# Kernel tuning notes

Measured on AMD Instinct MI355X. Metric: run time of the kernel, lower is better.

The kernel has to match this reference:

```python
import jax, jax.numpy as jnp
import numpy as np

B, L, D, H = 2, 2048, 1024, 16
HD = D // H  # 64


def rotate_half(x):
    x1, x2 = x[..., : x.shape[-1] // 2], x[..., x.shape[-1] // 2 :]
    return jnp.concatenate([-x2, x1], axis=-1)


def apply_rope(x, cos, sin):
    # x: (B, H, L, HD); cos/sin: (1, L, HD)
    c = cos[:, None, : x.shape[2], :]
    s = sin[:, None, : x.shape[2], :]
    return x * c + rotate_half(x) * s


def setup_inputs() -> dict:
    key = jax.random.key(0)
    ks = jax.random.split(key, 16)
    query = jax.random.normal(ks[0], (B, L, D), jnp.float32)
    k_in = jax.random.normal(ks[1], (B, L, D), jnp.float32)
    v_in = jax.random.normal(ks[2], (B, L, D), jnp.float32)
    key_padding_mask = jax.random.uniform(ks[3], (B, L)) < 0.2
    # genuine RoPE tables
    inv_freq = 1.0 / (10000.0 ** (jnp.arange(0, HD, 2, dtype=jnp.float32) / HD))
    ang = jnp.arange(L, dtype=jnp.float32)[:, None] * inv_freq[None, :]  # (L, HD/2)
    ang = jnp.concatenate([ang, ang], axis=-1)  # (L, HD)
    rope_cos = jnp.cos(ang)[None]  # (1, L, HD)
    rope_sin = jnp.sin(ang)[None]
    scale = 0.02
    Wq = jax.random.normal(ks[4], (D, D), jnp.float32) * scale
    bq = jnp.zeros((D,), jnp.float32)
    Wk = jax.random.normal(ks[5], (D, D), jnp.float32) * scale
    bk = jnp.zeros((D,), jnp.float32)
    Wv = jax.random.normal(ks[6], (D, D), jnp.float32) * scale
    bv = jnp.zeros((D,), jnp.float32)
    Wg = jax.random.normal(ks[7], (D, D), jnp.float32) * scale  # init zeros in torch; random for grad coverage
    bg = jnp.ones((D,), jnp.float32)
    Wo = jax.random.normal(ks[8], (D, D), jnp.float32) * scale
    bo = jnp.zeros((D,), jnp.float32)
    return dict(query=query, key=k_in, value=v_in, key_padding_mask=key_padding_mask,
                rope_cos=rope_cos, rope_sin=rope_sin,
                Wq=Wq, bq=bq, Wk=Wk, bk=bk, Wv=Wv, bv=bv,
                Wg=Wg, bg=bg, Wo=Wo, bo=bo)


def reference(query, key, value, key_padding_mask, rope_cos, rope_sin,
              Wq, bq, Wk, bk, Wv, bv, Wg, bg, Wo, bo):
    Bq, Lq, _ = query.shape
    Lk = key.shape[1]
    # torch Linear: x @ W.T + b
    Q = (query @ Wq.T + bq).reshape(Bq, Lq, H, HD).transpose(0, 2, 1, 3)
    K = (key @ Wk.T + bk).reshape(Bq, Lk, H, HD).transpose(0, 2, 1, 3)
    V = (value @ Wv.T + bv).reshape(Bq, Lk, H, HD).transpose(0, 2, 1, 3)
    K = apply_rope(K, rope_cos, rope_sin)
    Q = apply_rope(Q, rope_cos, rope_sin)
    scale = 1.0 / jnp.sqrt(jnp.asarray(HD, query.dtype))
    scores = jnp.einsum('bhqd,bhkd->bhqk', Q, K) * scale
    allow = ~key_padding_mask[:, None, None, :]  # (B,1,1,Lk): True = attend
    scores = jnp.where(allow, scores, -jnp.inf)
    attn = jax.nn.softmax(scores, axis=-1)
    out = jnp.einsum('bhqk,bhkd->bhqd', attn, V)
    out = jnp.nan_to_num(out, nan=0.0)
    out = out.transpose(0, 2, 1, 3).reshape(Bq, Lq, D)
    gate = jax.nn.sigmoid(query @ Wg.T + bg)
    out = out * gate
    out = out @ Wo.T + bo
    return out
```

## Files before the change

kernel.cpp:

```cpp
#include <hip/hip_runtime.h>
#include <hip/hip_bf16.h>
#include <cstdint>


constexpr int NB = 2, NL = 2048, ND = 1024, NH = 16, NHD = 64;
constexpr int NM = NB * NL;

typedef __bf16 bf16_t;
typedef __bf16 bf16x8 __attribute__((ext_vector_type(8)));
typedef __bf16 bf16x4 __attribute__((ext_vector_type(4)));
typedef float f32x4 __attribute__((ext_vector_type(4)));
typedef float f32x16 __attribute__((ext_vector_type(16)));
typedef unsigned int uint2v __attribute__((ext_vector_type(2)));

typedef const __attribute__((address_space(1))) void* gas_ptr;
typedef __attribute__((address_space(3))) void* las_ptr;

__device__ __forceinline__ void async_load16(const void* g, void* l) {
  __builtin_amdgcn_global_load_lds((gas_ptr)g, (las_ptr)l, 16, 0, 0);
}

__device__ __forceinline__ unsigned cvtpk_bf16(float lo, float hi) {
  unsigned r;
  asm("v_cvt_pk_bf16_f32 %0, %1, %2" : "=v"(r) : "v"(lo), "v"(hi));
  return r;
}

__device__ __forceinline__ void pl32_swap(unsigned& a, unsigned& b) {
#if __has_builtin(__builtin_amdgcn_permlane32_swap)
  uint2v r = __builtin_amdgcn_permlane32_swap(a, b, false, false);
  a = r.x; b = r.y;
#else
  asm volatile("v_permlane32_swap_b32 %0, %1" : "+v"(a), "+v"(b));
#endif
}

struct CvtArgs {
  const float* s[8];
  bf16_t* d[8];
};
__global__ __launch_bounds__(256) void cvt8_kernel(CvtArgs a) {
  int y = blockIdx.y;
  int n4 = (y < 3) ? (NM * ND / 4) : (ND * ND / 4);
  const float* src = a.s[y];
  bf16_t* dst = a.d[y];
  for (int i = blockIdx.x * 256 + threadIdx.x; i < n4; i += gridDim.x * 256) {
    float4 v = ((const float4*)src)[i];
    bf16x4 o;
    o[0] = (bf16_t)v.x; o[1] = (bf16_t)v.y; o[2] = (bf16_t)v.z; o[3] = (bf16_t)v.w;
    ((bf16x4*)dst)[i] = o;
  }
}

template <int MODE>
__global__ __launch_bounds__(256) void gemm_kernel(
    const bf16_t* __restrict__ Aq, const bf16_t* __restrict__ Ak, const bf16_t* __restrict__ Av,
    const bf16_t* __restrict__ W0, const bf16_t* __restrict__ W1,
    const bf16_t* __restrict__ W2, const bf16_t* __restrict__ W3,
    const float* __restrict__ b0, const float* __restrict__ b1,
    const float* __restrict__ b2, const float* __restrict__ b3,
    const float* __restrict__ ctab, const float* __restrict__ stab,
    bf16_t* __restrict__ Qr, bf16_t* __restrict__ Kr, bf16_t* __restrict__ Vt,
    bf16_t* __restrict__ Gb, float* __restrict__ Out) {
  __shared__ __align__(16) bf16_t lA[2][128 * 64];
  __shared__ __align__(16) bf16_t lB[2][128 * 64];
  const int tid = threadIdx.x, lane = tid & 63, w = tid >> 6;
  const int wm = w >> 1, wn = w & 1;
  const int lr = lane & 15, lg = lane >> 4;

  const int lin = blockIdx.x;
  const int xcd = lin & 7, idx = lin >> 3;
  constexpr int G = (MODE == 1) ? 4 : 1;
  const int ntile = xcd * G + (idx & (G - 1));
  const int mtile = idx / G;

  const bf16_t* Asrc;
  const bf16_t* Wsrc;
  int nofs, t = 0;
  if constexpr (MODE == 1) {
    t = ntile >> 3;
    Asrc = (t == 1) ? Ak : (t == 2) ? Av : Aq;
    Wsrc = (t == 0) ? W0 : (t == 1) ? W1 : (t == 2) ? W2 : W3;
    nofs = (ntile & 7) * 128;
  } else {
    Asrc = Aq; Wsrc = W0; nofs = ntile * 128;
  }
  const bf16_t* Ablk = Asrc + mtile * 128 * ND;
  const bf16_t* Wblk = Wsrc + nofs * ND;

  f32x4 acc[4][4];
#pragma unroll
  for (int i = 0; i < 4; ++i)
#pragma unroll
    for (int j = 0; j < 4; ++j)
#pragma unroll
      for (int k = 0; k < 4; ++k) acc[i][j][k] = 0.f;

  auto STAGE = [&](int b, int kb) {
#pragma unroll
    for (int p = 0; p < 4; ++p) {
      int q = w * 256 + p * 64 + lane;
      int r = q >> 3, c = q & 7;
      int cs = c ^ (r & 7);
      async_load16(Ablk + r * ND + kb * 64 + cs * 8, &lA[b][(w * 256 + p * 64) * 8]);
      async_load16(Wblk + r * ND + kb * 64 + cs * 8, &lB[b][(w * 256 + p * 64) * 8]);
    }
  };
  auto COMPUTE = [&](int b) {
    const bf16_t* pA = lA[b];
    const bf16_t* pB = lB[b];
#pragma unroll
    for (int ks = 0; ks < 2; ++ks) {
      bf16x8 af[4], bfr[4];
#pragma unroll
      for (int i = 0; i < 4; ++i) {
        int ra = wm * 64 + i * 16 + lr;
        int ca = (ks * 4 + lg) ^ (ra & 7);
        af[i] = *(const bf16x8*)(pA + ra * 64 + ca * 8);
        int rb = wn * 64 + i * 16 + lr;
        int cb = (ks * 4 + lg) ^ (rb & 7);
        bfr[i] = *(const bf16x8*)(pB + rb * 64 + cb * 8);
      }
#pragma unroll
      for (int i = 0; i < 4; ++i)
#pragma unroll
        for (int j = 0; j < 4; ++j)
          acc[i][j] = __builtin_amdgcn_mfma_f32_16x16x32_bf16(af[i], bfr[j], acc[i][j], 0, 0, 0);
    }
  };

  STAGE(0, 0);
  __syncthreads();
  int buf = 0;
  for (int kb = 0; kb < 15; ++kb) {
    STAGE(buf ^ 1, kb + 1);
    COMPUTE(buf);
    __syncthreads();
    buf ^= 1;
  }
  COMPUTE(buf);

  if constexpr (MODE == 0) {
#pragma unroll
    for (int j = 0; j < 4; ++j) {
      int nn = ntile * 128 + wn * 64 + j * 16 + lr;
      float bias = b0[nn];
#pragma unroll
      for (int i = 0; i < 4; ++i)
#pragma unroll
        for (int rg = 0; rg < 4; ++rg) {
          int mm = mtile * 128 + wm * 64 + i * 16 + lg * 4 + rg;
          Out[mm * ND + nn] = acc[i][j][rg] + bias;
        }
    }
  } else {
    const int fbase = nofs + wn * 64;
    const int h = fbase >> 6;
    if (t < 2) {
      bf16_t* dst = (t == 0) ? Qr : Kr;
      const float* bias = (t == 0) ? b0 : b1;
      const float qs = (t == 0) ? 0.18033688011112042f : 1.0f;
#pragma unroll
      for (int i = 0; i < 4; ++i)
#pragma unroll
        for (int rg = 0; rg < 4; ++rg) {
          int mm = mtile * 128 + wm * 64 + i * 16 + lg * 4 + rg;
          int bb = mm >> 11, l = mm & (NL - 1);
          bf16_t* rowp = dst + ((bb * NH + h) * NL + l) * NHD;
          const float* crow = ctab + l * NHD;
          const float* srow = stab + l * NHD;
#pragma unroll
          for (int j = 0; j < 2; ++j) {
            int dlo = j * 16 + lr, dhi = dlo + 32;
            float xlo = acc[i][j][rg] + bias[fbase + dlo];
            float xhi = acc[i][j + 2][rg] + bias[fbase + dhi];
            float olo = (xlo * crow[dlo] - xhi * srow[dlo]) * qs;
            float ohi = (xhi * crow[dhi] + xlo * srow[dhi]) * qs;
            rowp[dlo] = (bf16_t)olo;
            rowp[dhi] = (bf16_t)ohi;
          }
        }
    } else if (t == 2) {
#pragma unroll
      for (int i = 0; i < 4; ++i) {
        int mmb = mtile * 128 + wm * 64 + i * 16 + lg * 4;
        int bb = mmb >> 11, l0 = mmb & (NL - 1);
#pragma unroll
        for (int j = 0; j < 4; ++j) {
          int d = j * 16 + lr;
          float bias = b2[fbase + d];
          unsigned u01 = cvtpk_bf16(acc[i][j][0] + bias, acc[i][j][1] + bias);
          unsigned u23 = cvtpk_bf16(acc[i][j][2] + bias, acc[i][j][3] + bias);
          unsigned long long pk = (unsigned long long)u01 | ((unsigned long long)u23 << 32);
          *(unsigned long long*)(Vt + ((bb * NH + h) * NHD + d) * NL + l0) = pk;
        }
      }
    } else {
#pragma unroll
      for (int i = 0; i < 4; ++i)
#pragma unroll
        for (int rg = 0; rg < 4; ++rg) {
          int mm = mtile * 128 + wm * 64 + i * 16 + lg * 4 + rg;
#pragma unroll
          for (int j = 0; j < 4; ++j) {
            int f = fbase + j * 16 + lr;
            Gb[mm * ND + f] = (bf16_t)(acc[i][j][rg] + b3[f]);
          }
        }
    }
  }
}

__global__ __launch_bounds__(256) void attn_kernel(
    const bf16_t* __restrict__ Qr, const bf16_t* __restrict__ Kr, const bf16_t* __restrict__ Vt,
    const int* __restrict__ mask, const bf16_t* __restrict__ Gb, bf16_t* __restrict__ X) {
  __shared__ __align__(16) bf16_t lK[2][128 * 64];
  __shared__ __align__(16) bf16_t lV[2][64 * 128];

  int lin = blockIdx.y * gridDim.x + blockIdx.x;
  int swz = (lin & 7) * 64 + (lin >> 3);
  const int qb = swz & 15, bh = swz >> 4;
  const int bb = bh >> 4, h = bh & 15;

  const int tid = threadIdx.x, lane = tid & 63, w = tid >> 6;
  const int ql = lane & 31, hi = lane >> 5;

  const bf16_t* Kbh = Kr + bh * NL * NHD;
  const bf16_t* Vbh = Vt + bh * NHD * NL;
  const int q = qb * 128 + w * 32 + ql;

  const bf16_t* Qp = Qr + (bh * NL + q) * NHD + 8 * hi;
  bf16x8 qf[4];
#pragma unroll
  for (int c = 0; c < 4; ++c) qf[c] = *(const bf16x8*)(Qp + 16 * c);
  bf16x8 qf5 = {};
  qf5[0] = (bf16_t)(hi ? 0.f : 1.f);

  f32x16 acc[2];
#pragma unroll
  for (int dt = 0; dt < 2; ++dt)
#pragma unroll
    for (int r = 0; r < 16; ++r) acc[dt][r] = 0.f;
  float lrun = 0.f;

  const bf16_t* gsrc[8];
#pragma unroll
  for (int j = 0; j < 8; ++j) {
    if (j < 4) {
      int u = j * 256 + tid;
      int r = u >> 3, c = u & 7, cs = c ^ (r & 7);
      gsrc[j] = Kbh + r * NHD + cs * 8;
    } else {
      int v = (j - 4) * 256 + tid;
      int r = v >> 4, c = v & 15, cs = (c & 8) | ((c & 7) ^ (r & 7));
      gsrc[j] = Vbh + r * NL + cs * 8;
    }
  }
  auto STAGE = [&](int b) {
#pragma unroll
    for (int j = 0; j < 8; ++j) {
      if (j < 4) {
        async_load16(gsrc[j], &lK[b][(j * 256 + tid) * 8]);
        gsrc[j] += 128 * NHD;
      } else {
        async_load16(gsrc[j], &lV[b][((j - 4) * 256 + tid) * 8]);
        gsrc[j] += 128;
      }
    }
  };

  unsigned rdK[2][4], rdV[2][4];
#pragma unroll
  for (int t2 = 0; t2 < 2; ++t2)
#pragma unroll
    for (int c = 0; c < 4; ++c) {
      unsigned un = ((2 * c + hi) ^ (ql & 7)) * 16;
      rdK[t2][c] = (32 * t2 + ql) * 128 + un;
      rdV[t2][c] = (32 * t2 + ql) * 256 + un;
    }
  const char* lKc = (const char*)lK;
  const char* lVc = (const char*)lV;

  STAGE(0);
  int mv0 = mask[bb * NL + lane];
  int mv1 = mask[bb * NL + 64 + lane];
  __syncthreads();

  auto BODY = [&](int buf, int t) {
    int nmv0 = 0, nmv1 = 0;
    if (t < 15) {
      STAGE(buf ^ 1);
      nmv0 = mask[bb * NL + (t + 1) * 128 + lane];
      nmv1 = mask[bb * NL + (t + 1) * 128 + 64 + lane];
    }
    unsigned long long bmA = __ballot(mv0 != 0);
    unsigned long long bmB = __ballot(mv1 != 0);
    unsigned mws[4] = {(unsigned)bmA, (unsigned)(bmA >> 32),
                       (unsigned)bmB, (unsigned)(bmB >> 32)};
    bf16x8 kf5[4];
#pragma unroll
    for (int g = 0; g < 4; ++g) {
      float bv = ((mws[g] >> ql) & 1u) ? -1008.f : -8.f;
      bf16x8 z = {};
      z[0] = (bf16_t)(hi ? 0.f : bv);
      kf5[g] = z;
    }
    float ts[16];
#pragma unroll
    for (int hh = 0; hh < 2; ++hh) {
      f32x16 st[2];
      __builtin_amdgcn_s_setprio(1);
#pragma unroll
      for (int t2 = 0; t2 < 2; ++t2) {
        f32x16 s;
#pragma unroll
        for (int r = 0; r < 16; ++r) s[r] = 0.f;
#pragma unroll
        for (int c = 0; c < 4; ++c) {
          bf16x8 kf = *(const bf16x8*)(lKc + rdK[t2][c] + buf * 16384 + hh * 8192);
          s = __builtin_amdgcn_mfma_f32_32x32x16_bf16(kf, qf[c], s, 0, 0, 0);
        }
        s = __builtin_amdgcn_mfma_f32_32x32x16_bf16(kf5[hh * 2 + t2], qf5, s, 0, 0, 0);
        st[t2] = s;
      }
      __builtin_amdgcn_s_setprio(0);

#pragma unroll
      for (int t2 = 0; t2 < 2; ++t2)
#pragma unroll
        for (int r = 0; r < 16; ++r) st[t2][r] = exp2f(st[t2][r]);
#pragma unroll
      for (int r = 0; r < 16; ++r) {
        float v = st[0][r] + st[1][r];
        if (hh == 0) ts[r] = v; else ts[r] += v;
      }

      unsigned wds[2][4][2];
#pragma unroll
      for (int t2 = 0; t2 < 2; ++t2)
#pragma unroll
        for (int r1 = 0; r1 < 4; ++r1) {
          wds[t2][r1][0] = cvtpk_bf16(st[t2][4 * r1 + 0], st[t2][4 * r1 + 1]);
          wds[t2][r1][1] = cvtpk_bf16(st[t2][4 * r1 + 2], st[t2][4 * r1 + 3]);
        }
      bf16x8 pf[4];
#pragma unroll
      for (int kc = 0; kc < 4; ++kc) {
        int t2 = kc >> 1, r1a = 2 * (kc & 1);
        unsigned a0 = wds[t2][r1a][0], b0 = wds[t2][r1a + 1][0];
        unsigned a1 = wds[t2][r1a][1], b1 = wds[t2][r1a + 1][1];
        pl32_swap(a0, b0);
        pl32_swap(a1, b1);
        union { unsigned u[4]; bf16x8 v; } uu;
        uu.u[0] = a0; uu.u[1] = a1; uu.u[2] = b0; uu.u[3] = b1;
        pf[kc] = uu.v;
      }

      __builtin_amdgcn_s_setprio(1);
#pragma unroll
      for (int dt = 0; dt < 2; ++dt) {
        f32x16 a = acc[dt];
#pragma unroll
        for (int kc = 0; kc < 4; ++kc) {
          bf16x8 vf = *(const bf16x8*)(lVc + rdV[dt][kc] + buf * 16384 + hh * 128);
          a = __builtin_amdgcn_mfma_f32_32x32x16_bf16(vf, pf[kc], a, 0, 0, 0);
        }
        acc[dt] = a;
      }
      __builtin_amdgcn_s_setprio(0);
    }
#pragma unroll
    for (int off = 8; off > 0; off >>= 1)
#pragma unroll
      for (int r = 0; r < 8; ++r)
        if (r < off) ts[r] += ts[r + off];
    lrun += ts[0];
    __syncthreads();
    mv0 = nmv0;
    mv1 = nmv1;
  };

  for (int tt = 0; tt < 8; ++tt) {
    BODY(0, 2 * tt);
    BODY(1, 2 * tt + 1);
  }

  float lt = lrun + __shfl_xor(lrun, 32, 64);
  float rinv = lt > 0.f ? 1.f / lt : 0.f;
  const int rowbase = (bb * NL + q) * ND + h * NHD;
#pragma unroll
  for (int dt = 0; dt < 2; ++dt)
#pragma unroll
    for (int r1 = 0; r1 < 4; ++r1) {
      int dbase = 32 * dt + 8 * r1 + 4 * hi;
      bf16x4 g4 = *(const bf16x4*)(Gb + rowbase + dbase);
      bf16x4 o;
#pragma unroll
      for (int j = 0; j < 4; ++j) {
        float gate = 1.f / (1.f + exp2f(-1.44269504f * (float)g4[j]));
        o[j] = (bf16_t)(acc[dt][4 * r1 + j] * rinv * gate);
      }
      *(bf16x4*)(X + rowbase + dbase) = o;
    }
}

extern "C" void kernel_launch(void* const* d_in, const int* in_sizes, int n_in,
                              void* d_out, int out_size, void* d_ws, size_t ws_size,
                              hipStream_t stream) {
  const float* query = (const float*)d_in[0];
  const float* key   = (const float*)d_in[1];
  const float* value = (const float*)d_in[2];
  const int*   maskp = (const int*)d_in[3];
  const float* rcos  = (const float*)d_in[4];
  const float* rsin  = (const float*)d_in[5];
  const float* Wq = (const float*)d_in[6];  const float* bq = (const float*)d_in[7];
  const float* Wk = (const float*)d_in[8];  const float* bk = (const float*)d_in[9];
  const float* Wv = (const float*)d_in[10]; const float* bv = (const float*)d_in[11];
  const float* Wg = (const float*)d_in[12]; const float* bg = (const float*)d_in[13];
  const float* Wo = (const float*)d_in[14]; const float* bo = (const float*)d_in[15];

  constexpr size_t MB = 1ull << 20;
  char* ws = (char*)d_ws;
  bf16_t* qbb = (bf16_t*)(ws + 0 * MB);
  bf16_t* kbb = (bf16_t*)(ws + 8 * MB);
  bf16_t* vbb = (bf16_t*)(ws + 16 * MB);
  bf16_t* wqb = (bf16_t*)(ws + 24 * MB);
  bf16_t* wkb = (bf16_t*)(ws + 26 * MB);
  bf16_t* wvb = (bf16_t*)(ws + 28 * MB);
  bf16_t* wgb = (bf16_t*)(ws + 30 * MB);
  bf16_t* wob = (bf16_t*)(ws + 32 * MB);
  bf16_t* Qr  = (bf16_t*)(ws + 34 * MB);
  bf16_t* Kr  = (bf16_t*)(ws + 42 * MB);
  bf16_t* Vt  = (bf16_t*)(ws + 50 * MB);
  bf16_t* Gb  = (bf16_t*)(ws + 58 * MB);
  bf16_t* Xb  = (bf16_t*)(ws + 74 * MB);

  CvtArgs ca;
  ca.s[0] = query; ca.d[0] = qbb;
  ca.s[1] = key;   ca.d[1] = kbb;
  ca.s[2] = value; ca.d[2] = vbb;
  ca.s[3] = Wq;    ca.d[3] = wqb;
  ca.s[4] = Wk;    ca.d[4] = wkb;
  ca.s[5] = Wv;    ca.d[5] = wvb;
  ca.s[6] = Wg;    ca.d[6] = wgb;
  ca.s[7] = Wo;    ca.d[7] = wob;
  cvt8_kernel<<<dim3(1024, 8), 256, 0, stream>>>(ca);

  gemm_kernel<1><<<1024, 256, 0, stream>>>(
      qbb, kbb, vbb, wqb, wkb, wvb, wgb, bq, bk, bv, bg, rcos, rsin,
      Qr, Kr, Vt, Gb, nullptr);

  attn_kernel<<<dim3(16, 32), 256, 0, stream>>>(Qr, Kr, Vt, maskp, Gb, Xb);

  gemm_kernel<0><<<256, 256, 0, stream>>>(
      Xb, nullptr, nullptr, wob, nullptr, nullptr, nullptr,
      bo, nullptr, nullptr, nullptr, nullptr, nullptr,
      nullptr, nullptr, nullptr, nullptr, (float*)d_out);
}
```

Before: 152.8 us.

## Use 256x256-tile 8-wave pipelined GEMM for fused QKV/gate projection

Replaces the 128x128-tile, 4-wave projection GEMM with a 256x256-tile, 512-thread kernel using 128KB of dynamic LDS. Each of the 256 blocks handles a quarter-output slice for one of the Q/K/V/gate projections. Loads are staged in half-tiles interleaved with MFMA work, with explicit vmcnt waits, barriers and s_setprio raising wave priority around the MFMA bursts. The larger tile doubles reuse of global loads per output and cuts block count to one per CU. The cost is higher register and LDS pressure and more complex synchronization. The output-projection GEMM is split into its own simplified kernel with unchanged math.

```diff
diff --git a/kernel.cpp b/kernel.cpp
--- a/kernel.cpp
+++ b/kernel.cpp
@@ -52,8 +52,7 @@
   }
 }
 
-template <int MODE>
-__global__ __launch_bounds__(256) void gemm_kernel(
+__global__ __launch_bounds__(512, 2) void gemm8_kernel(
     const bf16_t* __restrict__ Aq, const bf16_t* __restrict__ Ak, const bf16_t* __restrict__ Av,
     const bf16_t* __restrict__ W0, const bf16_t* __restrict__ W1,
     const bf16_t* __restrict__ W2, const bf16_t* __restrict__ W3,
@@ -61,7 +60,178 @@
     const float* __restrict__ b2, const float* __restrict__ b3,
     const float* __restrict__ ctab, const float* __restrict__ stab,
     bf16_t* __restrict__ Qr, bf16_t* __restrict__ Kr, bf16_t* __restrict__ Vt,
-    bf16_t* __restrict__ Gb, float* __restrict__ Out) {
+    bf16_t* __restrict__ Gb) {
+  extern __shared__ __align__(16) bf16_t smem[];
+  bf16_t* lA = smem;
+  bf16_t* lB = smem + 32768;
+
+  const int tid = threadIdx.x, lane = tid & 63, w = tid >> 6;
+  const int wm = w >> 2, wn = w & 3;
+  const int lr = lane & 15, lg = lane >> 4;
+
+  const int lin = blockIdx.x;
+  const int xcd = lin & 7, idx = lin >> 3;
+  const int nt = xcd * 2 + (idx & 1);
+  const int mt = idx >> 1;
+  const int t = nt >> 2;
+  const bf16_t* Asrc = (t == 1) ? Ak : (t == 2) ? Av : Aq;
+  const bf16_t* Wsrc = (t == 0) ? W0 : (t == 1) ? W1 : (t == 2) ? W2 : W3;
+  const int nbase = (nt & 3) * 256;
+
+  const int srow = lane >> 3;
+  const int gcol = ((lane & 7) ^ srow) * 8;
+
+  auto stageA = [&](int buf, int hf, int kt) {
+#pragma unroll
+    for (int jj = 0; jj < 2; ++jj) {
+      int slot = jj * 8 + w;
+      int r = slot * 8 + srow;
+      async_load16(Asrc + (size_t)(mt * 256 + hf * 128 + r) * ND + kt * 64 + gcol,
+                   lA + (buf * 2 + hf) * 8192 + slot * 512);
+    }
+  };
+  auto stageB = [&](int buf, int hf, int kt) {
+#pragma unroll
+    for (int jj = 0; jj < 2; ++jj) {
+      int slot = jj * 8 + w;
+      int r = slot * 8 + srow;
+      async_load16(Wsrc + (size_t)(nbase + hf * 128 + r) * ND + kt * 64 + gcol,
+                   lB + (buf * 2 + hf) * 8192 + slot * 512);
+    }
+  };
+
+  f32x4 acc[8][4];
+#pragma unroll
+  for (int i = 0; i < 8; ++i)
+#pragma unroll
+    for (int j = 0; j < 4; ++j)
+#pragma unroll
+      for (int k = 0; k < 4; ++k) acc[i][j][k] = 0.f;
+
+  stageA(0, 0, 0); stageA(0, 1, 0); stageB(0, 0, 0); stageB(0, 1, 0);
+  stageB(1, 0, 1); stageB(1, 1, 1);
+  asm volatile("s_waitcnt vmcnt(4)" ::: "memory");
+  __builtin_amdgcn_s_barrier();
+
+  const bf16_t* Ab[2] = { lA + wm * 8192, lA + (2 + wm) * 8192 };
+  const bf16_t* Bb[2] = { lB + (wn >> 1) * 8192 + (wn & 1) * 4096,
+                          lB + (2 + (wn >> 1)) * 8192 + (wn & 1) * 4096 };
+
+  for (int j = 0; j < 8; ++j) {
+#pragma unroll
+    for (int hp = 0; hp < 2; ++hp) {
+      const bf16_t* Ap = Ab[hp];
+      const bf16_t* Bp = Bb[hp];
+      bf16x8 bfr[4][2];
+#pragma unroll
+      for (int p = 0; p < 4; ++p) {
+        bf16x8 af[2][2];
+#pragma unroll
+        for (int mi = 0; mi < 2; ++mi)
+#pragma unroll
+          for (int ks = 0; ks < 2; ++ks)
+            af[mi][ks] = *(const bf16x8*)(Ap + ((p * 2 + mi) * 16 + lr) * 64 +
+                                          ((ks * 4 + lg) ^ (lr & 7)) * 8);
+        if (p == 0) {
+#pragma unroll
+          for (int nj = 0; nj < 4; ++nj)
+#pragma unroll
+            for (int ks = 0; ks < 2; ++ks)
+              bfr[nj][ks] = *(const bf16x8*)(Bp + (nj * 16 + lr) * 64 +
+                                             ((ks * 4 + lg) ^ (lr & 7)) * 8);
+        }
+        if (hp == 0) {
+          if (p == 0) stageA(1, 0, 2 * j + 1);
+          if (p == 1) { stageA(1, 1, 2 * j + 1); if (j < 7) stageB(0, 0, 2 * j + 2); }
+          if (p == 2) { if (j < 7) stageB(0, 1, 2 * j + 2); }
+        } else if (j < 7) {
+          if (p == 0) stageA(0, 0, 2 * j + 2);
+          if (p == 1) { stageA(0, 1, 2 * j + 2); stageB(1, 0, 2 * j + 3); }
+          if (p == 2) stageB(1, 1, 2 * j + 3);
+        }
+        __builtin_amdgcn_s_barrier();
+        __builtin_amdgcn_s_setprio(1);
+#pragma unroll
+        for (int mi = 0; mi < 2; ++mi)
+#pragma unroll
+          for (int nj = 0; nj < 4; ++nj)
+#pragma unroll
+            for (int ks = 0; ks < 2; ++ks)
+              acc[p * 2 + mi][nj] = __builtin_amdgcn_mfma_f32_16x16x32_bf16(
+                  af[mi][ks], bfr[nj][ks], acc[p * 2 + mi][nj], 0, 0, 0);
+        __builtin_amdgcn_s_setprio(0);
+        if (p == 3) {
+          if (hp == 0) {
+            if (j < 7) { asm volatile("s_waitcnt vmcnt(4)" ::: "memory"); }
+            else       { asm volatile("s_waitcnt vmcnt(0)" ::: "memory"); }
+          } else if (j < 7) {
+            asm volatile("s_waitcnt vmcnt(4)" ::: "memory");
+          }
+        }
+        __builtin_amdgcn_s_barrier();
+      }
+    }
+  }
+
+  const int fbase = nbase + wn * 64;
+  const int h = fbase >> 6;
+  if (t < 2) {
+    bf16_t* dst = (t == 0) ? Qr : Kr;
+    const float* bias = (t == 0) ? b0 : b1;
+    const float qs = (t == 0) ? 0.18033688011112042f : 1.0f;
+#pragma unroll
+    for (int i = 0; i < 8; ++i)
+#pragma unroll
+      for (int rg = 0; rg < 4; ++rg) {
+        int mm = mt * 256 + wm * 128 + i * 16 + lg * 4 + rg;
+        int bb = mm >> 11, l = mm & (NL - 1);
+        bf16_t* rowp = dst + ((bb * NH + h) * NL + l) * NHD;
+        const float* crow = ctab + l * NHD;
+        const float* srw = stab + l * NHD;
+#pragma unroll
+        for (int nj = 0; nj < 2; ++nj) {
+          int dlo = nj * 16 + lr, dhi = dlo + 32;
+          float xlo = acc[i][nj][rg] + bias[fbase + dlo];
+          float xhi = acc[i][nj + 2][rg] + bias[fbase + dhi];
+          float olo = (xlo * crow[dlo] - xhi * srw[dlo]) * qs;
+          float ohi = (xhi * crow[dhi] + xlo * srw[dhi]) * qs;
+          rowp[dlo] = (bf16_t)olo;
+          rowp[dhi] = (bf16_t)ohi;
+        }
+      }
+  } else if (t == 2) {
+#pragma unroll
+    for (int i = 0; i < 8; ++i) {
+      int mmb = mt * 256 + wm * 128 + i * 16 + lg * 4;
+      int bb = mmb >> 11, l0 = mmb & (NL - 1);
+#pragma unroll
+      for (int nj = 0; nj < 4; ++nj) {
+        int d = nj * 16 + lr;
+        float bias = b2[fbase + d];
+        unsigned u01 = cvtpk_bf16(acc[i][nj][0] + bias, acc[i][nj][1] + bias);
+        unsigned u23 = cvtpk_bf16(acc[i][nj][2] + bias, acc[i][nj][3] + bias);
+        unsigned long long pk = (unsigned long long)u01 | ((unsigned long long)u23 << 32);
+        *(unsigned long long*)(Vt + ((bb * NH + h) * NHD + d) * NL + l0) = pk;
+      }
+    }
+  } else {
+#pragma unroll
+    for (int i = 0; i < 8; ++i)
+#pragma unroll
+      for (int rg = 0; rg < 4; ++rg) {
+        int mm = mt * 256 + wm * 128 + i * 16 + lg * 4 + rg;
+#pragma unroll
+        for (int nj = 0; nj < 4; ++nj) {
+          int f = fbase + nj * 16 + lr;
+          Gb[mm * ND + f] = (bf16_t)(acc[i][nj][rg] + b3[f]);
+        }
+      }
+  }
+}
+
+__global__ __launch_bounds__(256) void gemm_out_kernel(
+    const bf16_t* __restrict__ A, const bf16_t* __restrict__ W,
+    const float* __restrict__ bias0, float* __restrict__ Out) {
   __shared__ __align__(16) bf16_t lA[2][128 * 64];
   __shared__ __align__(16) bf16_t lB[2][128 * 64];
   const int tid = threadIdx.x, lane = tid & 63, w = tid >> 6;
@@ -69,24 +239,10 @@
   const int lr = lane & 15, lg = lane >> 4;
 
   const int lin = blockIdx.x;
-  const int xcd = lin & 7, idx = lin >> 3;
-  constexpr int G = (MODE == 1) ? 4 : 1;
-  const int ntile = xcd * G + (idx & (G - 1));
-  const int mtile = idx / G;
-
-  const bf16_t* Asrc;
-  const bf16_t* Wsrc;
-  int nofs, t = 0;
-  if constexpr (MODE == 1) {
-    t = ntile >> 3;
-    Asrc = (t == 1) ? Ak : (t == 2) ? Av : Aq;
-    Wsrc = (t == 0) ? W0 : (t == 1) ? W1 : (t == 2) ? W2 : W3;
-    nofs = (ntile & 7) * 128;
-  } else {
-    Asrc = Aq; Wsrc = W0; nofs = ntile * 128;
-  }
-  const bf16_t* Ablk = Asrc + mtile * 128 * ND;
-  const bf16_t* Wblk = Wsrc + nofs * ND;
+  const int ntile = lin & 7, mtile = lin >> 3;
+
+  const bf16_t* Ablk = A + mtile * 128 * ND;
+  const bf16_t* Wblk = W + ntile * 128 * ND;
 
   f32x4 acc[4][4];
 #pragma unroll
@@ -140,74 +296,17 @@
   }
   COMPUTE(buf);
 
-  if constexpr (MODE == 0) {
-#pragma unroll
-    for (int j = 0; j < 4; ++j) {
-      int nn = ntile * 128 + wn * 64 + j * 16 + lr;
-      float bias = b0[nn];
-#pragma unroll
-      for (int i = 0; i < 4; ++i)
-#pragma unroll
-        for (int rg = 0; rg < 4; ++rg) {
-          int mm = mtile * 128 + wm * 64 + i * 16 + lg * 4 + rg;
-          Out[mm * ND + nn] = acc[i][j][rg] + bias;
-        }
-    }
-  } else {
-    const int fbase = nofs + wn * 64;
-    const int h = fbase >> 6;
-    if (t < 2) {
-      bf16_t* dst = (t == 0) ? Qr : Kr;
-      const float* bias = (t == 0) ? b0 : b1;
-      const float qs = (t == 0) ? 0.18033688011112042f : 1.0f;
-#pragma unroll
-      for (int i = 0; i < 4; ++i)
-#pragma unroll
-        for (int rg = 0; rg < 4; ++rg) {
-          int mm = mtile * 128 + wm * 64 + i * 16 + lg * 4 + rg;
-          int bb = mm >> 11, l = mm & (NL - 1);
-          bf16_t* rowp = dst + ((bb * NH + h) * NL + l) * NHD;
-          const float* crow = ctab + l * NHD;
-          const float* srow = stab + l * NHD;
-#pragma unroll
-          for (int j = 0; j < 2; ++j) {
-            int dlo = j * 16 + lr, dhi = dlo + 32;
-            float xlo = acc[i][j][rg] + bias[fbase + dlo];
-            float xhi = acc[i][j + 2][rg] + bias[fbase + dhi];
-            float olo = (xlo * crow[dlo] - xhi * srow[dlo]) * qs;
-            float ohi = (xhi * crow[dhi] + xlo * srow[dhi]) * qs;
-            rowp[dlo] = (bf16_t)olo;
-            rowp[dhi] = (bf16_t)ohi;
-          }
-        }
-    } else if (t == 2) {
-#pragma unroll
-      for (int i = 0; i < 4; ++i) {
-        int mmb = mtile * 128 + wm * 64 + i * 16 + lg * 4;
-        int bb = mmb >> 11, l0 = mmb & (NL - 1);
-#pragma unroll
-        for (int j = 0; j < 4; ++j) {
-          int d = j * 16 + lr;
-          float bias = b2[fbase + d];
-          unsigned u01 = cvtpk_bf16(acc[i][j][0] + bias, acc[i][j][1] + bias);
-          unsigned u23 = cvtpk_bf16(acc[i][j][2] + bias, acc[i][j][3] + bias);
-          unsigned long long pk = (unsigned long long)u01 | ((unsigned long long)u23 << 32);
-          *(unsigned long long*)(Vt + ((bb * NH + h) * NHD + d) * NL + l0) = pk;
-        }
-      }
-    } else {
-#pragma unroll
-      for (int i = 0; i < 4; ++i)
-#pragma unroll
-        for (int rg = 0; rg < 4; ++rg) {
-          int mm = mtile * 128 + wm * 64 + i * 16 + lg * 4 + rg;
-#pragma unroll
-          for (int j = 0; j < 4; ++j) {
-            int f = fbase + j * 16 + lr;
-            Gb[mm * ND + f] = (bf16_t)(acc[i][j][rg] + b3[f]);
-          }
-        }
-    }
+#pragma unroll
+  for (int j = 0; j < 4; ++j) {
+    int nn = ntile * 128 + wn * 64 + j * 16 + lr;
+    float bias = bias0[nn];
+#pragma unroll
+    for (int i = 0; i < 4; ++i)
+#pragma unroll
+      for (int rg = 0; rg < 4; ++rg) {
+        int mm = mtile * 128 + wm * 64 + i * 16 + lg * 4 + rg;
+        Out[mm * ND + nn] = acc[i][j][rg] + bias;
+      }
   }
 }
 
@@ -446,14 +545,11 @@
   ca.s[7] = Wo;    ca.d[7] = wob;
   cvt8_kernel<<<dim3(1024, 8), 256, 0, stream>>>(ca);
 
-  gemm_kernel<1><<<1024, 256, 0, stream>>>(
+  gemm8_kernel<<<256, 512, 131072, stream>>>(
       qbb, kbb, vbb, wqb, wkb, wvb, wgb, bq, bk, bv, bg, rcos, rsin,
-      Qr, Kr, Vt, Gb, nullptr);
+      Qr, Kr, Vt, Gb);
 
   attn_kernel<<<dim3(16, 32), 256, 0, stream>>>(Qr, Kr, Vt, maskp, Gb, Xb);
 
-  gemm_kernel<0><<<256, 256, 0, stream>>>(
-      Xb, nullptr, nullptr, wob, nullptr, nullptr, nullptr,
-      bo, nullptr, nullptr, nullptr, nullptr, nullptr,
-      nullptr, nullptr, nullptr, nullptr, (float*)d_out);
-}
+  gemm_out_kernel<<<256, 256, 0, stream>>>(Xb, wob, bo, (float*)d_out);
+}
```

Measured after the change: 145.3 us. 4.9% less time.
